# Performance work log

Hardware: AMD Instinct MI355X
Metric: run time of the kernel (lower is better)

The kernel has to match this reference:

```python
import jax, jax.numpy as jnp
import numpy as np

NUM_NODES = 100000
NUM_EDGES = 3200000
D_IN, D_HID, D_OUT = 64, 64, 32


def setup_inputs() -> dict:
    key = jax.random.key(0)
    k1, k2, k3, k4, k5 = jax.random.split(key, 5)
    edge_index = jax.random.randint(k1, (2, NUM_EDGES), 0, NUM_NODES, dtype=jnp.int64)
    edge_weight = jax.random.uniform(k2, (NUM_EDGES,), dtype=jnp.float32)
    emb = jax.random.normal(k3, (NUM_NODES, D_IN), dtype=jnp.float32)
    # glorot-ish scaled weights for the two GCNConv layers
    W1 = jax.random.normal(k4, (D_IN, D_HID), dtype=jnp.float32) * (1.0 / np.sqrt(D_IN))
    b1 = jnp.zeros((D_HID,), dtype=jnp.float32)
    W2 = jax.random.normal(k5, (D_HID, D_OUT), dtype=jnp.float32) * (1.0 / np.sqrt(D_HID))
    b2 = jnp.zeros((D_OUT,), dtype=jnp.float32)
    return {"edge_index": edge_index, "edge_weight": edge_weight,
            "emb": emb, "W1": W1, "b1": b1, "W2": W2, "b2": b2}


def reference(edge_index, edge_weight, emb, W1, b1, W2, b2):
    N = emb.shape[0]
    row, col = edge_index[0], edge_index[1]
    # PyG gcn_norm: add self-loops (weight 1.0), symmetric normalization
    loop = jnp.arange(N, dtype=edge_index.dtype)
    row_f = jnp.concatenate([row, loop])
    col_f = jnp.concatenate([col, loop])
    ew_f = jnp.concatenate([edge_weight, jnp.ones((N,), dtype=edge_weight.dtype)])
    deg = jax.ops.segment_sum(ew_f, col_f, num_segments=N)          # [N]
    deg_inv_sqrt = jnp.where(deg > 0, jax.lax.rsqrt(deg), 0.0)      # inf -> 0
    norm = deg_inv_sqrt[row_f] * ew_f * deg_inv_sqrt[col_f]         # [E+N]

    def gcn_conv(x, W, b):
        x = x @ W                                                    # [N, d_out]
        msg = x[row_f] * norm[:, None]                               # [E+N, d_out]
        out = jax.ops.segment_sum(msg, col_f, num_segments=N)       # [N, d_out]
        return out + b

    x = jax.nn.relu(gcn_conv(emb, W1, b1))
    x = gcn_conv(x, W2, b2)
    # F.normalize(p=2, dim=1, eps=1e-12)
    l2 = jnp.linalg.norm(x, axis=1, keepdims=True)
    return x / jnp.maximum(l2, 1e-12)
```

## Files before the change

kernel.cpp:

```cpp
#include <hip/hip_runtime.h>
#include <hip/hip_fp16.h>
#include <math.h>

#define THREADS 256
#define P5THREADS 512
#define BWIDTH 512
#define BSHIFT 9
#define CHUNK 3125
#define G1ROWS 16
#define G2ROWS 16

__global__ void init_kernel(const int* __restrict__ ei32, int* __restrict__ flag,
                            unsigned int* __restrict__ gcnt) {
    int t = threadIdx.x;
    gcnt[t] = 0u;
    if (t == 0) {
        int z = (ei32[1] == 0) + (ei32[3] == 0) + (ei32[5] == 0) + (ei32[7] == 0);
        *flag = (z == 4) ? 1 : 0;
    }
}

__device__ __forceinline__ int edge_at(const void* ei, int is64, size_t idx) {
    return is64 ? (int)((const long long*)ei)[idx] : ((const int*)ei)[idx];
}

__device__ __forceinline__ float wdec(unsigned int v) {
    return __half2float(__ushort_as_half((unsigned short)(v & 0x7FFFu)));
}

__device__ __forceinline__ void acc8(float* acc, float w, int4 g) {
    float2 x0 = __half22float2(*(const __half2*)&g.x);
    float2 x1 = __half22float2(*(const __half2*)&g.y);
    float2 x2 = __half22float2(*(const __half2*)&g.z);
    float2 x3 = __half22float2(*(const __half2*)&g.w);
    acc[0] = fmaf(w, x0.x, acc[0]); acc[1] = fmaf(w, x0.y, acc[1]);
    acc[2] = fmaf(w, x1.x, acc[2]); acc[3] = fmaf(w, x1.y, acc[3]);
    acc[4] = fmaf(w, x2.x, acc[4]); acc[5] = fmaf(w, x2.y, acc[5]);
    acc[6] = fmaf(w, x3.x, acc[6]); acc[7] = fmaf(w, x3.y, acc[7]);
}

__global__ void p1_count_kernel(const void* __restrict__ ei, const int* __restrict__ flag,
                                unsigned int* __restrict__ gcnt, unsigned int* __restrict__ table,
                                int E, int B) {
    __shared__ unsigned int lcnt[256];
    int t = threadIdx.x, b = blockIdx.x;
    lcnt[t] = 0u;
    __syncthreads();
    int is64 = *flag;
    int base = b * CHUNK;
    int end = min(E, base + CHUNK);
    for (int e = base + t; e < end; e += THREADS) {
        int c = edge_at(ei, is64, (size_t)E + e);
        atomicAdd(&lcnt[c >> BSHIFT], 1u);
    }
    __syncthreads();
    if (t < B) table[(size_t)b * 256 + t] = atomicAdd(&gcnt[t], lcnt[t]);
}

__global__ void p2_scan_kernel(const unsigned int* __restrict__ gcnt,
                               unsigned int* __restrict__ bstart, int B, int E) {
    int t = threadIdx.x;
    unsigned int v = (t < B) ? gcnt[t] : 0u;
    unsigned int incl = v;
    int lane = t & 63, wid = t >> 6;
#pragma unroll
    for (int off = 1; off < 64; off <<= 1) {
        unsigned int x = __shfl_up(incl, off);
        if (lane >= off) incl += x;
    }
    __shared__ unsigned int ws4[4];
    if (lane == 63) ws4[wid] = incl;
    __syncthreads();
    unsigned int wb = 0;
    for (int w = 0; w < wid; ++w) wb += ws4[w];
    unsigned int excl = wb + incl - v;
    if (t < B) bstart[t] = excl;
    if (t == 0) bstart[B] = (unsigned int)E;
}

__global__ void p3_scatter_kernel(const void* __restrict__ ei, const float* __restrict__ ew,
                                  const int* __restrict__ flag,
                                  const unsigned int* __restrict__ bstart,
                                  const unsigned int* __restrict__ table,
                                  int2* __restrict__ out, int E, int B) {
    __shared__ int2 stage[CHUNK];
    __shared__ unsigned char lbin[CHUNK];
    __shared__ unsigned short perm[CHUNK];
    __shared__ unsigned int lcnt[256];
    __shared__ unsigned int lcur[256];
    __shared__ int shiftb[256];
    __shared__ unsigned int ws4[4];

    int t = threadIdx.x, b = blockIdx.x;
    lcnt[t] = 0u;
    __syncthreads();
    int is64 = *flag;
    int base = b * CHUNK;
    int end = min(E, base + CHUNK);
    int n = end - base;
    for (int i = t; i < n; i += THREADS) {
        int e = base + i;
        int r = edge_at(ei, is64, (size_t)e);
        int c = edge_at(ei, is64, (size_t)E + e);
        int bin = c >> BSHIFT;
        stage[i] = make_int2(r | ((c & (BWIDTH - 1)) << 17), __float_as_int(ew[e]));
        lbin[i] = (unsigned char)bin;
        atomicAdd(&lcnt[bin], 1u);
    }
    __syncthreads();
    unsigned int v = lcnt[t];
    unsigned int incl = v;
    int lane = t & 63, wid = t >> 6;
#pragma unroll
    for (int off = 1; off < 64; off <<= 1) {
        unsigned int x = __shfl_up(incl, off);
        if (lane >= off) incl += x;
    }
    if (lane == 63) ws4[wid] = incl;
    __syncthreads();
    unsigned int wb = 0;
    for (int w = 0; w < wid; ++w) wb += ws4[w];
    unsigned int excl = wb + incl - v;
    lcur[t] = excl;
    shiftb[t] = (t < B) ? ((int)(bstart[t] + table[(size_t)b * 256 + t]) - (int)excl) : 0;
    __syncthreads();
    for (int i = t; i < n; i += THREADS) {
        unsigned int pos = atomicAdd(&lcur[lbin[i]], 1u);
        perm[pos] = (unsigned short)i;
    }
    __syncthreads();
    for (int k = t; k < n; k += THREADS) {
        int i = perm[k];
        int bin = lbin[i];
        out[(size_t)(shiftb[bin] + k)] = stage[i];
    }
}

__global__ void p5_bucket_kernel(const int2* __restrict__ bucketed,
                                 const unsigned int* __restrict__ bstart,
                                 float* __restrict__ dinv, int* __restrict__ colptr,
                                 unsigned int* __restrict__ csrp, int N, int E) {
    __shared__ unsigned int cnt[BWIDTH];
    __shared__ float deg[BWIDTH];
    __shared__ unsigned int cur[BWIDTH];
    __shared__ unsigned int ws8[8];

    int t = threadIdx.x, b = blockIdx.x;
    cnt[t] = 0u;
    deg[t] = 0.f;
    __syncthreads();
    unsigned int s = bstart[b], e2 = bstart[b + 1];
    for (unsigned int j = s + t; j < e2; j += P5THREADS) {
        int2 v = bucketed[j];
        unsigned int cl = ((unsigned int)v.x) >> 17;
        atomicAdd(&cnt[cl], 1u);
        atomicAdd(&deg[cl], __int_as_float(v.y));
    }
    __syncthreads();
    unsigned int v = cnt[t];
    unsigned int incl = v;
    int lane = t & 63, wid = t >> 6;
#pragma unroll
    for (int off = 1; off < 64; off <<= 1) {
        unsigned int x = __shfl_up(incl, off);
        if (lane >= off) incl += x;
    }
    if (lane == 63) ws8[wid] = incl;
    __syncthreads();
    unsigned int wb = 0;
    for (int w = 0; w < wid; ++w) wb += ws8[w];
    unsigned int excl = wb + incl - v;
    int node = (b << BSHIFT) + t;
    float d = rsqrtf(deg[t] + 1.0f);
    if (node < N) { colptr[node] = (int)(s + excl); dinv[node] = d; }
    deg[t] = d;
    cur[t] = s + excl;
    __syncthreads();
    for (unsigned int j = s + t; j < e2; j += P5THREADS) {
        int2 v2 = bucketed[j];
        unsigned int cl = ((unsigned int)v2.x) >> 17;
        unsigned int pos = atomicAdd(&cur[cl], 1u);
        float w = __int_as_float(v2.y) * deg[cl];
        unsigned short hb = __half_as_ushort(__float2half_rn(w));
        csrp[pos] = (((unsigned int)v2.x & 0x1FFFFu) << 15) | (unsigned int)(hb & 0x7FFFu);
    }
    if (b == 0 && t == 0) colptr[N] = E;
}

__global__ void gemm1_kernel(const float* __restrict__ X, const float* __restrict__ W,
                             const float* __restrict__ dinv, __half* __restrict__ Y,
                             int N, int tiles) {
    __shared__ float Wl[64 * 64];
    __shared__ float Xl[G1ROWS * 64];
    int tid = threadIdx.x;
    for (int i = tid; i < 64 * 64; i += 256) Wl[i] = W[i];
    int wid = tid >> 6, c = tid & 63;
    __syncthreads();
    for (int tile = blockIdx.x; tile < tiles; tile += gridDim.x) {
        int base = tile * G1ROWS;
        for (int i = tid; i < G1ROWS * 64; i += 256) {
            int rr = base + (i >> 6);
            Xl[i] = (rr < N) ? X[(size_t)rr * 64 + (i & 63)] : 0.f;
        }
        __syncthreads();
#pragma unroll
        for (int rg = 0; rg < G1ROWS / 4; ++rg) {
            int r = rg * 4 + wid;
            int row = base + r;
            if (row < N) {
                float acc = 0.f;
#pragma unroll
                for (int k = 0; k < 64; ++k) acc = fmaf(Xl[r * 64 + k], Wl[k * 64 + c], acc);
                Y[(size_t)row * 64 + c] = __float2half(acc * dinv[row]);
            }
        }
        __syncthreads();
    }
}

__global__ void gemm2_kernel(const __half* __restrict__ H, const float* __restrict__ W,
                             const float* __restrict__ dinv, __half* __restrict__ Y,
                             int N, int tiles) {
    __shared__ float Wl[64 * 32];
    __shared__ float Xl[G2ROWS * 64];
    int tid = threadIdx.x;
    for (int i = tid; i < 64 * 32; i += 256) Wl[i] = W[i];
    int rg0 = tid >> 5, c = tid & 31;
    __syncthreads();
    for (int tile = blockIdx.x; tile < tiles; tile += gridDim.x) {
        int base = tile * G2ROWS;
        for (int i = tid; i < G2ROWS * 32; i += 256) {
            int rr = base + (i >> 5);
            int kk = (i & 31) << 1;
            float2 f = make_float2(0.f, 0.f);
            if (rr < N) f = __half22float2(*(const __half2*)(H + (size_t)rr * 64 + kk));
            Xl[(i >> 5) * 64 + kk] = f.x;
            Xl[(i >> 5) * 64 + kk + 1] = f.y;
        }
        __syncthreads();
#pragma unroll
        for (int rg = 0; rg < G2ROWS / 8; ++rg) {
            int r = rg * 8 + rg0;
            int row = base + r;
            if (row < N) {
                float acc = 0.f;
#pragma unroll
                for (int k = 0; k < 64; ++k) acc = fmaf(Xl[r * 64 + k], Wl[k * 32 + c], acc);
                Y[(size_t)row * 32 + c] = __float2half(acc * dinv[row]);
            }
        }
        __syncthreads();
    }
}

__global__ void agg1_kernel(const __half* __restrict__ X1, const int* __restrict__ colptr,
                            const unsigned int* __restrict__ csrp,
                            const float* __restrict__ dinv, const float* __restrict__ bias,
                            __half* __restrict__ H, int N) {
    int tid = threadIdx.x;
    int node = blockIdx.x * 4 + (tid >> 6);
    if (node >= N) return;
    int lane = tid & 63;
    int eo = lane >> 3;
    int dq = lane & 7;
    int s = colptr[node], e = colptr[node + 1];
    float acc[8] = {0.f, 0.f, 0.f, 0.f, 0.f, 0.f, 0.f, 0.f};
    int j = s;
    while (j + 16 <= e) {
        unsigned int v0 = __builtin_nontemporal_load(&csrp[j + eo]);
        unsigned int v1 = __builtin_nontemporal_load(&csrp[j + 8 + eo]);
        int r0 = (int)(v0 >> 15), r1 = (int)(v1 >> 15);
        int4 g0 = *(const int4*)(X1 + ((size_t)r0 << 6) + (dq << 3));
        int4 g1 = *(const int4*)(X1 + ((size_t)r1 << 6) + (dq << 3));
        acc8(acc, wdec(v0), g0);
        acc8(acc, wdec(v1), g1);
        j += 16;
    }
    for (; j < e; j += 8) {
        int jj = j + eo;
        unsigned int v = (jj < e) ? csrp[jj] : 0u;
        float w = (jj < e) ? wdec(v) : 0.f;
        int r = (int)(v >> 15);
        int4 g = *(const int4*)(X1 + ((size_t)r << 6) + (dq << 3));
        acc8(acc, w, g);
    }
#pragma unroll
    for (int k = 0; k < 8; ++k) {
        acc[k] += __shfl_xor(acc[k], 8);
        acc[k] += __shfl_xor(acc[k], 16);
        acc[k] += __shfl_xor(acc[k], 32);
    }
    if (eo == 0) {
        float di = dinv[node];
        int4 gs = *(const int4*)(X1 + ((size_t)node << 6) + (dq << 3));
        float4 b0 = *(const float4*)(bias + dq * 8);
        float4 b1 = *(const float4*)(bias + dq * 8 + 4);
        float2 x0 = __half22float2(*(const __half2*)&gs.x);
        float2 x1 = __half22float2(*(const __half2*)&gs.y);
        float2 x2 = __half22float2(*(const __half2*)&gs.z);
        float2 x3 = __half22float2(*(const __half2*)&gs.w);
        float a0 = fmaxf(b0.x + fmaf(di, x0.x, acc[0]), 0.f);
        float a1 = fmaxf(b0.y + fmaf(di, x0.y, acc[1]), 0.f);
        float a2 = fmaxf(b0.z + fmaf(di, x1.x, acc[2]), 0.f);
        float a3 = fmaxf(b0.w + fmaf(di, x1.y, acc[3]), 0.f);
        float a4 = fmaxf(b1.x + fmaf(di, x2.x, acc[4]), 0.f);
        float a5 = fmaxf(b1.y + fmaf(di, x2.y, acc[5]), 0.f);
        float a6 = fmaxf(b1.z + fmaf(di, x3.x, acc[6]), 0.f);
        float a7 = fmaxf(b1.w + fmaf(di, x3.y, acc[7]), 0.f);
        int4 o;
        *(__half2*)&o.x = __floats2half2_rn(a0, a1);
        *(__half2*)&o.y = __floats2half2_rn(a2, a3);
        *(__half2*)&o.z = __floats2half2_rn(a4, a5);
        *(__half2*)&o.w = __floats2half2_rn(a6, a7);
        *(int4*)(H + ((size_t)node << 6) + (dq << 3)) = o;
    }
}

__global__ void agg2_kernel(const __half* __restrict__ X2, const int* __restrict__ colptr,
                            const unsigned int* __restrict__ csrp,
                            const float* __restrict__ dinv, const float* __restrict__ bias,
                            float* __restrict__ out, int N) {
    int tid = threadIdx.x;
    int node = blockIdx.x * 4 + (tid >> 6);
    if (node >= N) return;
    int lane = tid & 63;
    int eo = lane >> 2;
    int dq = lane & 3;
    int s = colptr[node], e = colptr[node + 1];
    float acc[8] = {0.f, 0.f, 0.f, 0.f, 0.f, 0.f, 0.f, 0.f};
    int j = s;
    while (j + 16 <= e) {
        unsigned int v = __builtin_nontemporal_load(&csrp[j + eo]);
        int r = (int)(v >> 15);
        int4 g = *(const int4*)(X2 + ((size_t)r << 5) + (dq << 3));
        acc8(acc, wdec(v), g);
        j += 16;
    }
    if (j < e) {
        int jj = j + eo;
        unsigned int v = (jj < e) ? csrp[jj] : 0u;
        float w = (jj < e) ? wdec(v) : 0.f;
        int r = (int)(v >> 15);
        int4 g = *(const int4*)(X2 + ((size_t)r << 5) + (dq << 3));
        acc8(acc, w, g);
    }
#pragma unroll
    for (int k = 0; k < 8; ++k) {
        acc[k] += __shfl_xor(acc[k], 4);
        acc[k] += __shfl_xor(acc[k], 8);
        acc[k] += __shfl_xor(acc[k], 16);
        acc[k] += __shfl_xor(acc[k], 32);
    }
    float a[8];
    float ss = 0.f;
    {
        float di = dinv[node];
        int4 gs = *(const int4*)(X2 + ((size_t)node << 5) + (dq << 3));
        float4 b0 = *(const float4*)(bias + dq * 8);
        float4 b1 = *(const float4*)(bias + dq * 8 + 4);
        float2 x0 = __half22float2(*(const __half2*)&gs.x);
        float2 x1 = __half22float2(*(const __half2*)&gs.y);
        float2 x2 = __half22float2(*(const __half2*)&gs.z);
        float2 x3 = __half22float2(*(const __half2*)&gs.w);
        a[0] = b0.x + fmaf(di, x0.x, acc[0]);
        a[1] = b0.y + fmaf(di, x0.y, acc[1]);
        a[2] = b0.z + fmaf(di, x1.x, acc[2]);
        a[3] = b0.w + fmaf(di, x1.y, acc[3]);
        a[4] = b1.x + fmaf(di, x2.x, acc[4]);
        a[5] = b1.y + fmaf(di, x2.y, acc[5]);
        a[6] = b1.z + fmaf(di, x3.x, acc[6]);
        a[7] = b1.w + fmaf(di, x3.y, acc[7]);
#pragma unroll
        for (int k = 0; k < 8; ++k) ss = fmaf(a[k], a[k], ss);
    }
    ss += __shfl_xor(ss, 1);
    ss += __shfl_xor(ss, 2);
    float inv = 1.f / fmaxf(sqrtf(ss), 1e-12f);
    if (eo == 0) {
        float4 o0 = make_float4(a[0] * inv, a[1] * inv, a[2] * inv, a[3] * inv);
        float4 o1 = make_float4(a[4] * inv, a[5] * inv, a[6] * inv, a[7] * inv);
        *(float4*)(out + ((size_t)node << 5) + (dq << 3)) = o0;
        *(float4*)(out + ((size_t)node << 5) + (dq << 3) + 4) = o1;
    }
}

extern "C" void kernel_launch(void* const* d_in, const int* in_sizes, int n_in,
                              void* d_out, int out_size, void* d_ws, size_t ws_size,
                              hipStream_t stream) {
    const void* ei = d_in[0];
    const float* ew = (const float*)d_in[1];
    const float* emb = (const float*)d_in[2];
    const float* W1 = (const float*)d_in[3];
    const float* b1 = (const float*)d_in[4];
    const float* W2 = (const float*)d_in[5];
    const float* b2 = (const float*)d_in[6];
    float* outp = (float*)d_out;

    int E = in_sizes[0] / 2;
    int N = in_sizes[2] / 64;
    int B = (N + BWIDTH - 1) >> BSHIFT;
    int GP = (E + CHUNK - 1) / CHUNK;

    char* p = (char*)d_ws;
    auto alloc = [&](size_t bytes) {
        void* q = (void*)p;
        p += (bytes + 255) & ~(size_t)255;
        return q;
    };
    unsigned int* gcnt   = (unsigned int*)alloc(256 * 4);
    unsigned int* bstart = (unsigned int*)alloc(257 * 4);
    int*          flag   = (int*)alloc(256);
    unsigned int* table  = (unsigned int*)alloc((size_t)GP * 256 * 4);
    int2*   bucketed = (int2*)alloc((size_t)E * 8);
    unsigned int* csrp = (unsigned int*)alloc(((size_t)E + 64) * 4);
    float*  dinv     = (float*)alloc((size_t)N * 4);
    int*    colptr   = (int*)alloc(((size_t)N + 1) * 4);
    __half* X1h      = (__half*)alloc((size_t)N * 64 * 2);
    __half* H        = (__half*)alloc((size_t)N * 64 * 2);
    __half* X2h      = X1h;

    int tiles1 = (N + G1ROWS - 1) / G1ROWS;
    int tiles2 = (N + G2ROWS - 1) / G2ROWS;

    init_kernel<<<1, 256, 0, stream>>>((const int*)ei, flag, gcnt);
    p1_count_kernel<<<GP, THREADS, 0, stream>>>(ei, flag, gcnt, table, E, B);
    p2_scan_kernel<<<1, 256, 0, stream>>>(gcnt, bstart, B, E);
    p3_scatter_kernel<<<GP, THREADS, 0, stream>>>(ei, ew, flag, bstart, table,
                                                  bucketed, E, B);
    p5_bucket_kernel<<<B, P5THREADS, 0, stream>>>(bucketed, bstart, dinv, colptr, csrp, N, E);
    gemm1_kernel<<<1024, THREADS, 0, stream>>>(emb, W1, dinv, X1h, N, tiles1);
    agg1_kernel<<<(N + 3) / 4, THREADS, 0, stream>>>(X1h, colptr, csrp, dinv, b1, H, N);
    gemm2_kernel<<<1024, THREADS, 0, stream>>>(H, W2, dinv, X2h, N, tiles2);
    agg2_kernel<<<(N + 3) / 4, THREADS, 0, stream>>>(X2h, colptr, csrp, dinv, b2, outp, N);
}
```

Baseline: 288.0 us.

## Fuse layer-2 GEMM into layer-1 aggregation epilogue with register-held W2

Removes the separate gemm2 kernel. The first aggregation kernel now multiplies each ReLU'd hidden row by W2 in registers: each lane holds an 8x4 slice of W2, and partial sums are reduced with warp shuffles before writing the 32-wide fp16 X2 row. This avoids writing and re-reading the 64-wide H buffer and saves a kernel launch. Each wavefront now loops over 16 nodes instead of one, which cuts the grid size and may reduce latency hiding for the gathers.

```diff
diff --git a/kernel.cpp b/kernel.cpp
--- a/kernel.cpp
+++ b/kernel.cpp
@@ -8,7 +8,7 @@
 #define BSHIFT 9
 #define CHUNK 3125
 #define G1ROWS 16
-#define G2ROWS 16
+#define NPW 16
 
 __global__ void init_kernel(const int* __restrict__ ei32, int* __restrict__ flag,
                             unsigned int* __restrict__ gcnt) {
@@ -218,101 +218,89 @@
     }
 }
 
-__global__ void gemm2_kernel(const __half* __restrict__ H, const float* __restrict__ W,
-                             const float* __restrict__ dinv, __half* __restrict__ Y,
-                             int N, int tiles) {
-    __shared__ float Wl[64 * 32];
-    __shared__ float Xl[G2ROWS * 64];
+__global__ void agg1_fused_kernel(const __half* __restrict__ X1, const int* __restrict__ colptr,
+                                  const unsigned int* __restrict__ csrp,
+                                  const float* __restrict__ dinv, const float* __restrict__ bias,
+                                  const float* __restrict__ W2, __half* __restrict__ X2,
+                                  int N) {
     int tid = threadIdx.x;
-    for (int i = tid; i < 64 * 32; i += 256) Wl[i] = W[i];
-    int rg0 = tid >> 5, c = tid & 31;
-    __syncthreads();
-    for (int tile = blockIdx.x; tile < tiles; tile += gridDim.x) {
-        int base = tile * G2ROWS;
-        for (int i = tid; i < G2ROWS * 32; i += 256) {
-            int rr = base + (i >> 5);
-            int kk = (i & 31) << 1;
-            float2 f = make_float2(0.f, 0.f);
-            if (rr < N) f = __half22float2(*(const __half2*)(H + (size_t)rr * 64 + kk));
-            Xl[(i >> 5) * 64 + kk] = f.x;
-            Xl[(i >> 5) * 64 + kk + 1] = f.y;
-        }
-        __syncthreads();
-#pragma unroll
-        for (int rg = 0; rg < G2ROWS / 8; ++rg) {
-            int r = rg * 8 + rg0;
-            int row = base + r;
-            if (row < N) {
-                float acc = 0.f;
-#pragma unroll
-                for (int k = 0; k < 64; ++k) acc = fmaf(Xl[r * 64 + k], Wl[k * 32 + c], acc);
-                Y[(size_t)row * 32 + c] = __float2half(acc * dinv[row]);
-            }
-        }
-        __syncthreads();
-    }
-}
-
-__global__ void agg1_kernel(const __half* __restrict__ X1, const int* __restrict__ colptr,
-                            const unsigned int* __restrict__ csrp,
-                            const float* __restrict__ dinv, const float* __restrict__ bias,
-                            __half* __restrict__ H, int N) {
-    int tid = threadIdx.x;
-    int node = blockIdx.x * 4 + (tid >> 6);
-    if (node >= N) return;
     int lane = tid & 63;
     int eo = lane >> 3;
     int dq = lane & 7;
-    int s = colptr[node], e = colptr[node + 1];
-    float acc[8] = {0.f, 0.f, 0.f, 0.f, 0.f, 0.f, 0.f, 0.f};
-    int j = s;
-    while (j + 16 <= e) {
-        unsigned int v0 = __builtin_nontemporal_load(&csrp[j + eo]);
-        unsigned int v1 = __builtin_nontemporal_load(&csrp[j + 8 + eo]);
-        int r0 = (int)(v0 >> 15), r1 = (int)(v1 >> 15);
-        int4 g0 = *(const int4*)(X1 + ((size_t)r0 << 6) + (dq << 3));
-        int4 g1 = *(const int4*)(X1 + ((size_t)r1 << 6) + (dq << 3));
-        acc8(acc, wdec(v0), g0);
-        acc8(acc, wdec(v1), g1);
-        j += 16;
-    }
-    for (; j < e; j += 8) {
-        int jj = j + eo;
-        unsigned int v = (jj < e) ? csrp[jj] : 0u;
-        float w = (jj < e) ? wdec(v) : 0.f;
-        int r = (int)(v >> 15);
-        int4 g = *(const int4*)(X1 + ((size_t)r << 6) + (dq << 3));
-        acc8(acc, w, g);
-    }
-#pragma unroll
-    for (int k = 0; k < 8; ++k) {
-        acc[k] += __shfl_xor(acc[k], 8);
-        acc[k] += __shfl_xor(acc[k], 16);
-        acc[k] += __shfl_xor(acc[k], 32);
-    }
-    if (eo == 0) {
+    float4 w2r[8];
+#pragma unroll
+    for (int kk = 0; kk < 8; ++kk)
+        w2r[kk] = *(const float4*)(W2 + (size_t)(8 * dq + kk) * 32 + 4 * eo);
+    float4 b0 = *(const float4*)(bias + dq * 8);
+    float4 b1 = *(const float4*)(bias + dq * 8 + 4);
+
+    int base = blockIdx.x * (4 * NPW) + (tid >> 6) * NPW;
+    for (int i = 0; i < NPW; ++i) {
+        int node = base + i;
+        if (node >= N) return;
+        int s = colptr[node], e = colptr[node + 1];
+        float acc[8] = {0.f, 0.f, 0.f, 0.f, 0.f, 0.f, 0.f, 0.f};
+        int j = s;
+        while (j + 16 <= e) {
+            unsigned int v0 = __builtin_nontemporal_load(&csrp[j + eo]);
+            unsigned int v1 = __builtin_nontemporal_load(&csrp[j + 8 + eo]);
+            int r0 = (int)(v0 >> 15), r1 = (int)(v1 >> 15);
+            int4 g0 = *(const int4*)(X1 + ((size_t)r0 << 6) + (dq << 3));
+            int4 g1 = *(const int4*)(X1 + ((size_t)r1 << 6) + (dq << 3));
+            acc8(acc, wdec(v0), g0);
+            acc8(acc, wdec(v1), g1);
+            j += 16;
+        }
+        for (; j < e; j += 8) {
+            int jj = j + eo;
+            unsigned int v = (jj < e) ? csrp[jj] : 0u;
+            float w = (jj < e) ? wdec(v) : 0.f;
+            int r = (int)(v >> 15);
+            int4 g = *(const int4*)(X1 + ((size_t)r << 6) + (dq << 3));
+            acc8(acc, w, g);
+        }
+#pragma unroll
+        for (int k = 0; k < 8; ++k) {
+            acc[k] += __shfl_xor(acc[k], 8);
+            acc[k] += __shfl_xor(acc[k], 16);
+            acc[k] += __shfl_xor(acc[k], 32);
+        }
         float di = dinv[node];
         int4 gs = *(const int4*)(X1 + ((size_t)node << 6) + (dq << 3));
-        float4 b0 = *(const float4*)(bias + dq * 8);
-        float4 b1 = *(const float4*)(bias + dq * 8 + 4);
         float2 x0 = __half22float2(*(const __half2*)&gs.x);
         float2 x1 = __half22float2(*(const __half2*)&gs.y);
         float2 x2 = __half22float2(*(const __half2*)&gs.z);
         float2 x3 = __half22float2(*(const __half2*)&gs.w);
-        float a0 = fmaxf(b0.x + fmaf(di, x0.x, acc[0]), 0.f);
-        float a1 = fmaxf(b0.y + fmaf(di, x0.y, acc[1]), 0.f);
-        float a2 = fmaxf(b0.z + fmaf(di, x1.x, acc[2]), 0.f);
-        float a3 = fmaxf(b0.w + fmaf(di, x1.y, acc[3]), 0.f);
-        float a4 = fmaxf(b1.x + fmaf(di, x2.x, acc[4]), 0.f);
-        float a5 = fmaxf(b1.y + fmaf(di, x2.y, acc[5]), 0.f);
-        float a6 = fmaxf(b1.z + fmaf(di, x3.x, acc[6]), 0.f);
-        float a7 = fmaxf(b1.w + fmaf(di, x3.y, acc[7]), 0.f);
-        int4 o;
-        *(__half2*)&o.x = __floats2half2_rn(a0, a1);
-        *(__half2*)&o.y = __floats2half2_rn(a2, a3);
-        *(__half2*)&o.z = __floats2half2_rn(a4, a5);
-        *(__half2*)&o.w = __floats2half2_rn(a6, a7);
-        *(int4*)(H + ((size_t)node << 6) + (dq << 3)) = o;
+        float h[8];
+        h[0] = fmaxf(b0.x + fmaf(di, x0.x, acc[0]), 0.f);
+        h[1] = fmaxf(b0.y + fmaf(di, x0.y, acc[1]), 0.f);
+        h[2] = fmaxf(b0.z + fmaf(di, x1.x, acc[2]), 0.f);
+        h[3] = fmaxf(b0.w + fmaf(di, x1.y, acc[3]), 0.f);
+        h[4] = fmaxf(b1.x + fmaf(di, x2.x, acc[4]), 0.f);
+        h[5] = fmaxf(b1.y + fmaf(di, x2.y, acc[5]), 0.f);
+        h[6] = fmaxf(b1.z + fmaf(di, x3.x, acc[6]), 0.f);
+        h[7] = fmaxf(b1.w + fmaf(di, x3.y, acc[7]), 0.f);
+        float y0 = 0.f, y1 = 0.f, y2 = 0.f, y3 = 0.f;
+#pragma unroll
+        for (int kk = 0; kk < 8; ++kk) {
+            y0 = fmaf(h[kk], w2r[kk].x, y0);
+            y1 = fmaf(h[kk], w2r[kk].y, y1);
+            y2 = fmaf(h[kk], w2r[kk].z, y2);
+            y3 = fmaf(h[kk], w2r[kk].w, y3);
+        }
+#pragma unroll
+        for (int m = 1; m <= 4; m <<= 1) {
+            y0 += __shfl_xor(y0, m);
+            y1 += __shfl_xor(y1, m);
+            y2 += __shfl_xor(y2, m);
+            y3 += __shfl_xor(y3, m);
+        }
+        if (dq == 0) {
+            int2 o;
+            *(__half2*)&o.x = __floats2half2_rn(y0 * di, y1 * di);
+            *(__half2*)&o.y = __floats2half2_rn(y2 * di, y3 * di);
+            *(int2*)(X2 + ((size_t)node << 5) + (eo << 2)) = o;
+        }
     }
 }
 
@@ -416,11 +404,9 @@
     float*  dinv     = (float*)alloc((size_t)N * 4);
     int*    colptr   = (int*)alloc(((size_t)N + 1) * 4);
     __half* X1h      = (__half*)alloc((size_t)N * 64 * 2);
-    __half* H        = (__half*)alloc((size_t)N * 64 * 2);
-    __half* X2h      = X1h;
+    __half* X2h      = (__half*)alloc((size_t)N * 32 * 2);
 
     int tiles1 = (N + G1ROWS - 1) / G1ROWS;
-    int tiles2 = (N + G2ROWS - 1) / G2ROWS;
 
     init_kernel<<<1, 256, 0, stream>>>((const int*)ei, flag, gcnt);
     p1_count_kernel<<<GP, THREADS, 0, stream>>>(ei, flag, gcnt, table, E, B);
@@ -429,7 +415,7 @@
                                                   bucketed, E, B);
     p5_bucket_kernel<<<B, P5THREADS, 0, stream>>>(bucketed, bstart, dinv, colptr, csrp, N, E);
     gemm1_kernel<<<1024, THREADS, 0, stream>>>(emb, W1, dinv, X1h, N, tiles1);
-    agg1_kernel<<<(N + 3) / 4, THREADS, 0, stream>>>(X1h, colptr, csrp, dinv, b1, H, N);
-    gemm2_kernel<<<1024, THREADS, 0, stream>>>(H, W2, dinv, X2h, N, tiles2);
+    agg1_fused_kernel<<<(N + 4 * NPW - 1) / (4 * NPW), THREADS, 0, stream>>>(
+        X1h, colptr, csrp, dinv, b1, W2, X2h, N);
     agg2_kernel<<<(N + 3) / 4, THREADS, 0, stream>>>(X2h, colptr, csrp, dinv, b2, outp, N);
 }
```

Result: slower. 309.2 us (+7.4%).
